# Kernel tuning notes

Hardware: AMD Instinct MI355X
Metric: run time of the kernel (lower is better)

Reference implementation:

```python
import jax, jax.numpy as jnp
import numpy as np

CAPACITY_FACTOR = 1.25


def setup_inputs() -> dict:
    key = jax.random.key(0)
    ks = jax.random.split(key, 5)
    B, N, D, E, H = 4, 2048, 1024, 8, 4096
    x = jax.random.normal(ks[0], (B, N, D), dtype=jnp.float32)
    w_router = jax.random.normal(ks[1], (D, E), dtype=jnp.float32) * 0.02
    w1 = jax.random.normal(ks[2], (E, D, H), dtype=jnp.float32) * 0.02
    b1 = jnp.zeros((E, H), dtype=jnp.float32)
    w2 = jax.random.normal(ks[3], (E, H, D), dtype=jnp.float32) * 0.02
    b2 = jnp.zeros((E, D), dtype=jnp.float32)
    return {"x": x, "w_router": w_router, "w1": w1, "b1": b1, "w2": w2, "b2": b2}


def reference(x, w_router, w1, b1, w2, b2):
    B, N, D = x.shape
    E = w_router.shape[1]
    C = int(N * CAPACITY_FACTOR // E)  # expert capacity

    # ---- top-1 switch router ----
    logits = jnp.einsum('bnd,de->bne', x, w_router)                 # [B,N,E]
    z = jax.nn.logsumexp(logits, axis=-1)                           # [B,N]
    router_z_loss = jnp.mean(z * z)
    probs = jax.nn.softmax(logits, axis=-1)                         # [B,N,E]
    gate = jnp.max(probs, axis=-1)                                  # [B,N]
    idx = jnp.argmax(probs, axis=-1)                                # [B,N]
    mask = jax.nn.one_hot(idx, E, dtype=x.dtype)                    # [B,N,E]

    # load-balancing aux loss (Switch-Transformer style)
    density = jnp.mean(mask, axis=1)                                # [B,E] fraction routed
    density_proxy = jnp.mean(probs, axis=1)                         # [B,E] mean router prob
    aux_loss = jnp.mean(jnp.sum(density * density_proxy, axis=-1)) * (E * E)

    # position within each expert; drop tokens beyond capacity
    pos = jnp.cumsum(mask, axis=1) - 1.0                            # [B,N,E]
    pos = pos.astype(jnp.int32)
    # one_hot zeros out indices outside [0,C); mask zeros unrouted slots
    dispatch = mask[..., None] * jax.nn.one_hot(pos, C, dtype=x.dtype)  # [B,N,E,C]
    combine = dispatch * gate[:, :, None, None]                     # [B,N,E,C]

    # ---- dense dispatch -> grouped expert FFN -> dense combine ----
    expert_inputs = jnp.einsum('bnd,bnec->becd', x, dispatch)       # [B,E,C,D]
    h = jax.nn.gelu(jnp.einsum('becd,edh->bech', expert_inputs, w1)
                    + b1[None, :, None, :])                          # [B,E,C,H]
    expert_outputs = jnp.einsum('bech,ehd->becd', h, w2) + b2[None, :, None, :]
    output = jnp.einsum('becd,bnec->bnd', expert_outputs, combine)  # [B,N,D]
    return output, aux_loss, router_z_loss
```

## Files before the change

### kernel.cpp

```cpp
#include <hip/hip_runtime.h>
#include <hip/hip_bf16.h>
#include <math.h>

#define B_ 4
#define N_ 2048
#define D_ 1024
#define E_ 8
#define H_ 4096
#define C_ 320
#define M_ (B_*C_)

typedef __attribute__((ext_vector_type(8))) short short8;
typedef __attribute__((ext_vector_type(4))) float floatx4;

__device__ __forceinline__ unsigned short f2bf(float f) {
  unsigned u = __builtin_bit_cast(unsigned, f);
  u += 0x7fffu + ((u >> 16) & 1u);
  return (unsigned short)(u >> 16);
}

__device__ __forceinline__ float gelu_fast(float x) {
  float u = 0.7978845608028654f * (x + 0.044715f * x * x * x);
  float t = 1.f - 2.f / (__expf(2.f * u) + 1.f);
  return 0.5f * x * (1.f + t);
}

__device__ __forceinline__ void gload_lds16(const unsigned short* g, unsigned short* l) {
  __builtin_amdgcn_global_load_lds(
      (const __attribute__((address_space(1))) unsigned int*)g,
      (__attribute__((address_space(3))) unsigned int*)l, 16, 0, 0);
}

__global__ __launch_bounds__(256) void router_kernel(
    const float* __restrict__ x, const float* __restrict__ wr,
    int* __restrict__ idx_buf, float* __restrict__ gate_buf,
    float* __restrict__ stats)
{
  int lane  = threadIdx.x & 63;
  int wave  = threadIdx.x >> 6;
  int token = blockIdx.x * 4 + wave;
  int b     = token >> 11;

  const float* xp = x + (size_t)token * D_ + lane * 16;
  float xv[16];
#pragma unroll
  for (int i = 0; i < 4; i++) {
    float4 v = ((const float4*)xp)[i];
    xv[i*4+0]=v.x; xv[i*4+1]=v.y; xv[i*4+2]=v.z; xv[i*4+3]=v.w;
  }
  double acc[8];
#pragma unroll
  for (int e = 0; e < 8; e++) acc[e] = 0.0;
  const float* wp = wr + (size_t)(lane * 16) * E_;
#pragma unroll
  for (int i = 0; i < 16; i++) {
    float xs = xv[i];
#pragma unroll
    for (int e = 0; e < 8; e++) acc[e] += (double)xs * (double)wp[i*8 + e];
  }
  for (int off = 32; off > 0; off >>= 1) {
#pragma unroll
    for (int e = 0; e < 8; e++) acc[e] += __shfl_xor(acc[e], off, 64);
  }

  float l[8];
#pragma unroll
  for (int e = 0; e < 8; e++) l[e] = (float)acc[e];
  float m = l[0]; int best = 0;
#pragma unroll
  for (int e = 1; e < 8; e++) if (l[e] > m) { m = l[e]; best = e; }
  float p[8], sum = 0.f;
#pragma unroll
  for (int e = 0; e < 8; e++) { p[e] = expf(l[e] - m); sum += p[e]; }
  float inv = 1.f / sum;
#pragma unroll
  for (int e = 0; e < 8; e++) p[e] *= inv;
  float z    = m + logf(sum);
  float gate = inv;

  __shared__ float s_cnt[8], s_prox[8], s_zsq[1];
  if (threadIdx.x < 8)  { s_cnt[threadIdx.x] = 0.f; s_prox[threadIdx.x] = 0.f; }
  if (threadIdx.x == 8) s_zsq[0] = 0.f;
  __syncthreads();
  if (lane == 0) {
    idx_buf[token]  = best;
    gate_buf[token] = gate;
    atomicAdd(&s_zsq[0], z * z);
    atomicAdd(&s_cnt[best], 1.f);
#pragma unroll
    for (int e = 0; e < 8; e++) atomicAdd(&s_prox[e], p[e]);
  }
  __syncthreads();
  if (threadIdx.x < 8) {
    atomicAdd(&stats[b*8 + threadIdx.x],      s_cnt[threadIdx.x]);
    atomicAdd(&stats[32 + b*8 + threadIdx.x], s_prox[threadIdx.x]);
  }
  if (threadIdx.x == 8) atomicAdd(&stats[64], s_zsq[0]);
}

__global__ __launch_bounds__(64) void pos_kernel(
    const int* __restrict__ idx_buf, int* __restrict__ slot_token)
{
  int be = blockIdx.x;
  int b = be >> 3, e = be & 7;
  int lane = threadIdx.x;
  int base = 0;
  int* out = slot_token + (size_t)(e * B_ + b) * C_;
  for (int n0 = 0; n0 < N_; n0 += 64) {
    int n = n0 + lane;
    bool match = (idx_buf[b * N_ + n] == e);
    unsigned long long mask = __ballot(match);
    int my = base + __popcll(mask & ((1ull << lane) - 1ull));
    if (match && my < C_) out[my] = b * N_ + n;
    base += __popcll(mask);
  }
}

__global__ __launch_bounds__(256) void gather_kernel(
    const float* __restrict__ x, const int* __restrict__ slot_token,
    unsigned short* __restrict__ xe)
{
  int row = blockIdx.x;
  int t = slot_token[row];
  int col = threadIdx.x * 4;
  ushort4 o;
  if (t >= 0) {
    float4 v = *(const float4*)(x + (size_t)t * D_ + col);
    o.x = f2bf(v.x); o.y = f2bf(v.y); o.z = f2bf(v.z); o.w = f2bf(v.w);
  } else {
    o.x = 0; o.y = 0; o.z = 0; o.w = 0;
  }
  *(ushort4*)(xe + (size_t)row * D_ + col) = o;
}

__global__ __launch_bounds__(256) void transcast_kernel(
    const float* __restrict__ in, unsigned short* __restrict__ out, int R, int Cc)
{
  int e = blockIdx.z;
  const float* pin = in + (size_t)e * R * Cc;
  unsigned short* pout = out + (size_t)e * R * Cc;
  __shared__ float T[32][33];
  int r0 = blockIdx.y * 32, c0 = blockIdx.x * 32;
  {
    int lr = threadIdx.x >> 3, lc4 = (threadIdx.x & 7) * 4;
    float4 v = *(const float4*)(pin + (size_t)(r0 + lr) * Cc + c0 + lc4);
    T[lr][lc4+0] = v.x; T[lr][lc4+1] = v.y; T[lr][lc4+2] = v.z; T[lr][lc4+3] = v.w;
  }
  __syncthreads();
  {
    int oc = threadIdx.x >> 3, or4 = (threadIdx.x & 7) * 4;
    ushort4 o;
    o.x = f2bf(T[or4+0][oc]); o.y = f2bf(T[or4+1][oc]);
    o.z = f2bf(T[or4+2][oc]); o.w = f2bf(T[or4+3][oc]);
    *(ushort4*)(pout + (size_t)(c0 + oc) * R + r0 + or4) = o;
  }
}

template<int EPI>
__global__ __launch_bounds__(256) void gemm_kernel(
    const unsigned short* __restrict__ A,
    const unsigned short* __restrict__ BT,
    const float* __restrict__ bias,
    unsigned short* __restrict__ Hout,
    float* __restrict__ Out,
    const int* __restrict__ slot_token,
    const float* __restrict__ gate_buf,
    int M, int K, int Nn)
{
  int e  = blockIdx.z;
  int m0 = blockIdx.y * 128;
  int n0 = blockIdx.x * 128;
  const unsigned short* Ae = A  + (size_t)e * M  * K;
  const unsigned short* Be = BT + (size_t)e * Nn * K;

  __shared__ __align__(16) unsigned short As[128 * 32];
  __shared__ __align__(16) unsigned short Bs[128 * 32];
  __shared__ int   s_tok[128];
  __shared__ float s_gate[128];

  int tid  = threadIdx.x;
  int lane = tid & 63;
  int wave = tid >> 6;
  int wm   = (wave >> 1) * 64;
  int wn   = (wave & 1) * 64;
  int lr   = lane & 15;
  int quad = lane >> 4;

  if constexpr (EPI == 1) {
    if (tid < 128) {
      int t = slot_token[(size_t)e * M + m0 + tid];
      s_tok[tid]  = t;
      s_gate[tid] = (t >= 0) ? gate_buf[t] : 0.f;
    }
  }

  floatx4 acc[4][4];
#pragma unroll
  for (int i = 0; i < 4; i++)
#pragma unroll
    for (int j = 0; j < 4; j++) acc[i][j] = (floatx4){0.f, 0.f, 0.f, 0.f};

  int rA0 = wave * 32 + (lane >> 2);
  int kcc = (lane & 3) * 8;
  const unsigned short* Agp0 = Ae + (size_t)(m0 + rA0)      * K + kcc;
  const unsigned short* Agp1 = Ae + (size_t)(m0 + rA0 + 16) * K + kcc;
  const unsigned short* Bgp0 = Be + (size_t)(n0 + rA0)      * K + kcc;
  const unsigned short* Bgp1 = Be + (size_t)(n0 + rA0 + 16) * K + kcc;
  unsigned short* ldsA0 = &As[(wave * 32) * 32];
  unsigned short* ldsA1 = &As[(wave * 32 + 16) * 32];
  unsigned short* ldsB0 = &Bs[(wave * 32) * 32];
  unsigned short* ldsB1 = &Bs[(wave * 32 + 16) * 32];

  for (int k0 = 0; k0 < K; k0 += 32) {
    __syncthreads();
    gload_lds16(Agp0, ldsA0);
    gload_lds16(Agp1, ldsA1);
    gload_lds16(Bgp0, ldsB0);
    gload_lds16(Bgp1, ldsB1);
    Agp0 += 32; Agp1 += 32; Bgp0 += 32; Bgp1 += 32;
    __syncthreads();
    short8 af[4], bf[4];
#pragma unroll
    for (int i = 0; i < 4; i++) {
      af[i] = *(const short8*)(&As[(wm + i * 16 + lr) * 32 + quad * 8]);
      bf[i] = *(const short8*)(&Bs[(wn + i * 16 + lr) * 32 + quad * 8]);
    }
#pragma unroll
    for (int i = 0; i < 4; i++)
#pragma unroll
      for (int j = 0; j < 4; j++)
        acc[i][j] = __builtin_amdgcn_mfma_f32_16x16x32_bf16(af[i], bf[j], acc[i][j], 0, 0, 0);
  }

#pragma unroll
  for (int i = 0; i < 4; i++) {
    int rloc = wm + i * 16 + quad * 4;
#pragma unroll
    for (int j = 0; j < 4; j++) {
      int col = n0 + wn + j * 16 + lr;
      float bz = bias[(size_t)e * Nn + col];
      if constexpr (EPI == 0) {
        size_t base = (size_t)e * M * Nn + (size_t)(m0 + rloc) * Nn + col;
#pragma unroll
        for (int r = 0; r < 4; r++)
          Hout[base + (size_t)r * Nn] = f2bf(gelu_fast(acc[i][j][r] + bz));
      } else {
#pragma unroll
        for (int r = 0; r < 4; r++) {
          int t = s_tok[rloc + r];
          if (t >= 0)
            Out[(size_t)t * D_ + col] = s_gate[rloc + r] * (acc[i][j][r] + bz);
        }
      }
    }
  }
}

__global__ void loss_kernel(const float* __restrict__ stats, float* __restrict__ out)
{
  float aux = 0.f;
  for (int i = 0; i < 32; i++) aux += stats[i] * stats[32 + i];
  aux *= 64.f / ((float)B_ * (float)N_ * (float)N_);
  out[0] = aux;
  out[1] = stats[64] / (float)(B_ * N_);
}

extern "C" void kernel_launch(void* const* d_in, const int* in_sizes, int n_in,
                              void* d_out, int out_size, void* d_ws, size_t ws_size,
                              hipStream_t stream)
{
  (void)in_sizes; (void)n_in; (void)ws_size;
  const float* x  = (const float*)d_in[0];
  const float* wr = (const float*)d_in[1];
  const float* w1 = (const float*)d_in[2];
  const float* b1 = (const float*)d_in[3];
  const float* w2 = (const float*)d_in[4];
  const float* b2 = (const float*)d_in[5];
  float* out = (float*)d_out;

  char* ws = (char*)d_ws;
  int*   idx_buf  = (int*)(ws + 0);
  float* gate_buf = (float*)(ws + 32768);
  float* stats    = (float*)(ws + 65536);
  int*   slot_tok = (int*)(ws + 66560);
  unsigned short* xe  = (unsigned short*)(ws + 107520);
  unsigned short* wbf = (unsigned short*)(ws + 21079040);
  unsigned short* hbf = (unsigned short*)(ws + 88187904);

  hipMemsetAsync(d_out, 0, (size_t)out_size * 4, stream);
  hipMemsetAsync(stats, 0, 1024, stream);
  hipMemsetAsync(slot_tok, 0xFF, (size_t)E_ * B_ * C_ * 4, stream);

  router_kernel<<<(B_ * N_) / 4, 256, 0, stream>>>(x, wr, idx_buf, gate_buf, stats);
  pos_kernel<<<B_ * E_, 64, 0, stream>>>(idx_buf, slot_tok);
  gather_kernel<<<E_ * M_, 256, 0, stream>>>(x, slot_tok, xe);

  transcast_kernel<<<dim3(H_ / 32, D_ / 32, E_), 256, 0, stream>>>(w1, wbf, D_, H_);
  gemm_kernel<0><<<dim3(H_ / 128, M_ / 128, E_), 256, 0, stream>>>(
      xe, wbf, b1, hbf, nullptr, nullptr, nullptr, M_, D_, H_);
  transcast_kernel<<<dim3(D_ / 32, H_ / 32, E_), 256, 0, stream>>>(w2, wbf, H_, D_);
  gemm_kernel<1><<<dim3(D_ / 128, M_ / 128, E_), 256, 0, stream>>>(
      hbf, wbf, b2, nullptr, out, slot_tok, gate_buf, M_, H_, D_);

  loss_kernel<<<1, 1, 0, stream>>>(stats, out + (size_t)B_ * N_ * D_);
}
```

Baseline: 685.3 us.

## Double-buffer GEMM LDS tiles and enlarge weight transpose-cast tiles

The expert GEMM now keeps two LDS buffers per operand. Each iteration issues the global-to-LDS loads for the next K-slice before running the MFMAs on the current slice, which removes one barrier per iteration and overlaps memory latency with compute. Separately, the fp32-to-bf16 weight transpose kernel moves from 32x32 to 64x64 tiles with four loads and stores per thread, cutting block count and launch overhead. The cost is doubled LDS for the GEMM operand tiles and a larger shared tile in the transpose, which may reduce occupancy.

```diff
diff --git a/kernel.cpp b/kernel.cpp
--- a/kernel.cpp
+++ b/kernel.cpp
@@ -139,20 +139,30 @@
   int e = blockIdx.z;
   const float* pin = in + (size_t)e * R * Cc;
   unsigned short* pout = out + (size_t)e * R * Cc;
-  __shared__ float T[32][33];
-  int r0 = blockIdx.y * 32, c0 = blockIdx.x * 32;
+  __shared__ float T[64][65];
+  int r0 = blockIdx.y * 64, c0 = blockIdx.x * 64;
   {
-    int lr = threadIdx.x >> 3, lc4 = (threadIdx.x & 7) * 4;
-    float4 v = *(const float4*)(pin + (size_t)(r0 + lr) * Cc + c0 + lc4);
-    T[lr][lc4+0] = v.x; T[lr][lc4+1] = v.y; T[lr][lc4+2] = v.z; T[lr][lc4+3] = v.w;
+    int row = threadIdx.x >> 2;
+    int cb  = (threadIdx.x & 3) * 4;
+#pragma unroll
+    for (int p = 0; p < 4; p++) {
+      int col = cb + p * 16;
+      float4 v = *(const float4*)(pin + (size_t)(r0 + row) * Cc + c0 + col);
+      T[row][col+0] = v.x; T[row][col+1] = v.y; T[row][col+2] = v.z; T[row][col+3] = v.w;
+    }
   }
   __syncthreads();
   {
-    int oc = threadIdx.x >> 3, or4 = (threadIdx.x & 7) * 4;
-    ushort4 o;
-    o.x = f2bf(T[or4+0][oc]); o.y = f2bf(T[or4+1][oc]);
-    o.z = f2bf(T[or4+2][oc]); o.w = f2bf(T[or4+3][oc]);
-    *(ushort4*)(pout + (size_t)(c0 + oc) * R + r0 + or4) = o;
+    int ocb = threadIdx.x >> 4;
+    int or4 = (threadIdx.x & 15) * 4;
+#pragma unroll
+    for (int p = 0; p < 4; p++) {
+      int oc = ocb + p * 16;
+      ushort4 o;
+      o.x = f2bf(T[or4+0][oc]); o.y = f2bf(T[or4+1][oc]);
+      o.z = f2bf(T[or4+2][oc]); o.w = f2bf(T[or4+3][oc]);
+      *(ushort4*)(pout + (size_t)(c0 + oc) * R + r0 + or4) = o;
+    }
   }
 }
 
@@ -173,8 +183,8 @@
   const unsigned short* Ae = A  + (size_t)e * M  * K;
   const unsigned short* Be = BT + (size_t)e * Nn * K;
 
-  __shared__ __align__(16) unsigned short As[128 * 32];
-  __shared__ __align__(16) unsigned short Bs[128 * 32];
+  __shared__ __align__(16) unsigned short As[2][128 * 32];
+  __shared__ __align__(16) unsigned short Bs[2][128 * 32];
   __shared__ int   s_tok[128];
   __shared__ float s_gate[128];
 
@@ -202,34 +212,42 @@
 
   int rA0 = wave * 32 + (lane >> 2);
   int kcc = (lane & 3) * 8;
-  const unsigned short* Agp0 = Ae + (size_t)(m0 + rA0)      * K + kcc;
-  const unsigned short* Agp1 = Ae + (size_t)(m0 + rA0 + 16) * K + kcc;
-  const unsigned short* Bgp0 = Be + (size_t)(n0 + rA0)      * K + kcc;
-  const unsigned short* Bgp1 = Be + (size_t)(n0 + rA0 + 16) * K + kcc;
-  unsigned short* ldsA0 = &As[(wave * 32) * 32];
-  unsigned short* ldsA1 = &As[(wave * 32 + 16) * 32];
-  unsigned short* ldsB0 = &Bs[(wave * 32) * 32];
-  unsigned short* ldsB1 = &Bs[(wave * 32 + 16) * 32];
-
-  for (int k0 = 0; k0 < K; k0 += 32) {
+  const unsigned short* Ag0 = Ae + (size_t)(m0 + rA0)      * K + kcc;
+  const unsigned short* Ag1 = Ae + (size_t)(m0 + rA0 + 16) * K + kcc;
+  const unsigned short* Bg0 = Be + (size_t)(n0 + rA0)      * K + kcc;
+  const unsigned short* Bg1 = Be + (size_t)(n0 + rA0 + 16) * K + kcc;
+  const unsigned offA0 = (wave * 32) * 32;
+  const unsigned offA1 = (wave * 32 + 16) * 32;
+
+  gload_lds16(Ag0, &As[0][offA0]);
+  gload_lds16(Ag1, &As[0][offA1]);
+  gload_lds16(Bg0, &Bs[0][offA0]);
+  gload_lds16(Bg1, &Bs[0][offA1]);
+  Ag0 += 32; Ag1 += 32; Bg0 += 32; Bg1 += 32;
+
+  int nIter = K >> 5;
+  int buf = 0;
+  for (int it = 0; it < nIter; ++it) {
     __syncthreads();
-    gload_lds16(Agp0, ldsA0);
-    gload_lds16(Agp1, ldsA1);
-    gload_lds16(Bgp0, ldsB0);
-    gload_lds16(Bgp1, ldsB1);
-    Agp0 += 32; Agp1 += 32; Bgp0 += 32; Bgp1 += 32;
-    __syncthreads();
+    if (it + 1 < nIter) {
+      gload_lds16(Ag0, &As[buf ^ 1][offA0]);
+      gload_lds16(Ag1, &As[buf ^ 1][offA1]);
+      gload_lds16(Bg0, &Bs[buf ^ 1][offA0]);
+      gload_lds16(Bg1, &Bs[buf ^ 1][offA1]);
+      Ag0 += 32; Ag1 += 32; Bg0 += 32; Bg1 += 32;
+    }
     short8 af[4], bf[4];
 #pragma unroll
     for (int i = 0; i < 4; i++) {
-      af[i] = *(const short8*)(&As[(wm + i * 16 + lr) * 32 + quad * 8]);
-      bf[i] = *(const short8*)(&Bs[(wn + i * 16 + lr) * 32 + quad * 8]);
+      af[i] = *(const short8*)(&As[buf][(wm + i * 16 + lr) * 32 + quad * 8]);
+      bf[i] = *(const short8*)(&Bs[buf][(wn + i * 16 + lr) * 32 + quad * 8]);
     }
 #pragma unroll
     for (int i = 0; i < 4; i++)
 #pragma unroll
       for (int j = 0; j < 4; j++)
         acc[i][j] = __builtin_amdgcn_mfma_f32_16x16x32_bf16(af[i], bf[j], acc[i][j], 0, 0, 0);
+    buf ^= 1;
   }
 
 #pragma unroll
@@ -295,10 +313,10 @@
   pos_kernel<<<B_ * E_, 64, 0, stream>>>(idx_buf, slot_tok);
   gather_kernel<<<E_ * M_, 256, 0, stream>>>(x, slot_tok, xe);
 
-  transcast_kernel<<<dim3(H_ / 32, D_ / 32, E_), 256, 0, stream>>>(w1, wbf, D_, H_);
+  transcast_kernel<<<dim3(H_ / 64, D_ / 64, E_), 256, 0, stream>>>(w1, wbf, D_, H_);
   gemm_kernel<0><<<dim3(H_ / 128, M_ / 128, E_), 256, 0, stream>>>(
       xe, wbf, b1, hbf, nullptr, nullptr, nullptr, M_, D_, H_);
-  transcast_kernel<<<dim3(D_ / 32, H_ / 32, E_), 256, 0, stream>>>(w2, wbf, H_, D_);
+  transcast_kernel<<<dim3(D_ / 64, H_ / 64, E_), 256, 0, stream>>>(w2, wbf, H_, D_);
   gemm_kernel<1><<<dim3(D_ / 128, M_ / 128, E_), 256, 0, stream>>>(
       hbf, wbf, b2, nullptr, out, slot_tok, gate_buf, M_, H_, D_);
 
```

After: 673.4 us. About the same (-1.7%).
